# Optimization experiments

Hardware: AMD Instinct MI355X
Metric: run time of the kernel (lower is better)

The kernel has to match this reference:

```python
import jax, jax.numpy as jnp
import numpy as np

L, E, NH, V, BS = 8, 1024, 16, 32000, 1024  # layers, embed, heads, vocab, block_size
HD = E // NH  # head dim = 64
FF = 4 * E


def layernorm(x, scale, bias, eps=1e-5):
    mu = jnp.mean(x, axis=-1, keepdims=True)
    var = jnp.var(x, axis=-1, keepdims=True)
    return (x - mu) * jax.lax.rsqrt(var + eps) * scale + bias


def setup_inputs() -> dict:
    key = jax.random.key(0)
    ks = jax.random.split(key, 16)
    s = 0.02
    B, T = 2, 1024
    return {
        "idx": jax.random.randint(ks[0], (B, T), 0, V),
        "tok_emb": jax.random.normal(ks[1], (V, E), jnp.float32) * s,
        "pos_emb": jax.random.normal(ks[2], (BS, E), jnp.float32) * s,
        "Wq": jax.random.normal(ks[3], (L, E, E), jnp.float32) * s,
        "Wk": jax.random.normal(ks[4], (L, E, E), jnp.float32) * s,
        "Wv": jax.random.normal(ks[5], (L, E, E), jnp.float32) * s,
        "Wo": jax.random.normal(ks[6], (L, E, E), jnp.float32) * s,
        "bo": jnp.zeros((L, E), jnp.float32),
        "ln1_s": jnp.ones((L, E), jnp.float32),
        "ln1_b": jnp.zeros((L, E), jnp.float32),
        "W1": jax.random.normal(ks[7], (L, E, FF), jnp.float32) * s,
        "b1": jnp.zeros((L, FF), jnp.float32),
        "W2": jax.random.normal(ks[8], (L, FF, E), jnp.float32) * s,
        "b2": jnp.zeros((L, E), jnp.float32),
        "ln2_s": jnp.ones((L, E), jnp.float32),
        "ln2_b": jnp.zeros((L, E), jnp.float32),
        "lnf_s": jnp.ones((E,), jnp.float32),
        "lnf_b": jnp.zeros((E,), jnp.float32),
        "lm_w": jax.random.normal(ks[9], (E, V), jnp.float32) * s,
        "lm_b": jnp.zeros((V,), jnp.float32),
    }


def reference(idx, tok_emb, pos_emb, Wq, Wk, Wv, Wo, bo, ln1_s, ln1_b,
              W1, b1, W2, b2, ln2_s, ln2_b, lnf_s, lnf_b, lm_w, lm_b):
    B, T = idx.shape
    x = tok_emb[idx] + pos_emb[:T]  # [B,T,E]
    causal = jnp.triu(jnp.ones((T, T), bool), 1)  # True above diagonal -> masked
    scale = 1.0 / jnp.sqrt(jnp.asarray(HD, x.dtype))
    for l in range(L):
        h = layernorm(x, ln1_s[l], ln1_b[l])
        q = (h @ Wq[l]).reshape(B, T, NH, HD)
        k = (h @ Wk[l]).reshape(B, T, NH, HD)
        v = (h @ Wv[l]).reshape(B, T, NH, HD)
        scores = jnp.einsum("bthd,bshd->bhts", q, k) * scale  # [B,H,T,T]
        scores = jnp.where(causal, -jnp.inf, scores)
        attn = jax.nn.softmax(scores, axis=-1)
        o = jnp.einsum("bhts,bshd->bthd", attn, v).reshape(B, T, E)
        x = x + o @ Wo[l] + bo[l]
        h2 = layernorm(x, ln2_s[l], ln2_b[l])
        x = x + jax.nn.gelu(h2 @ W1[l] + b1[l], approximate=False) @ W2[l] + b2[l]
    x = layernorm(x, lnf_s, lnf_b)
    logits = x @ lm_w + lm_b  # [B,T,V]
    return logits
```

## Files before the change

### kernel.cpp

```cpp
#include <hip/hip_runtime.h>

#define EDIM 1024
#define NHEADS 16
#define HDIM 64
#define TSEQ 1024
#define NBATCH 2
#define MROWS 2048
#define FFDIM 4096
#define NLAYERS 8
#define VOCAB 32000
#define QKVN 3072

typedef __attribute__((ext_vector_type(4))) float f32x4;
typedef __attribute__((ext_vector_type(8))) short short8;

__device__ __forceinline__ unsigned short f2bf(float f) {
    union { float f; unsigned u; } v; v.f = f;
    unsigned r = v.u + 0x7fffu + ((v.u >> 16) & 1u);
    return (unsigned short)(r >> 16);
}

__device__ __forceinline__ f32x4 mfma_bf16(short8 a, short8 b, f32x4 c) {
    return __builtin_amdgcn_mfma_f32_16x16x32_bf16(a, b, c, 0, 0, 0);
}

__device__ __forceinline__ void gload16(const unsigned short* g, unsigned short* l) {
    __builtin_amdgcn_global_load_lds(
        (const __attribute__((address_space(1))) unsigned int*)g,
        (__attribute__((address_space(3))) unsigned int*)l, 16, 0, 0);
}

__global__ __launch_bounds__(256) void embed_kernel(
    const int* __restrict__ idx, const float* __restrict__ tok,
    const float* __restrict__ pos, float* __restrict__ x)
{
    int row = blockIdx.x;
    int t = row & (TSEQ - 1);
    int tokid = idx[row];
    const float* tp = tok + (size_t)tokid * EDIM;
    const float* pp = pos + (size_t)t * EDIM;
    float* xp = x + (size_t)row * EDIM;
    int c = threadIdx.x * 4;
    f32x4 a = *(const f32x4*)(tp + c);
    f32x4 b = *(const f32x4*)(pp + c);
    *(f32x4*)(xp + c) = a + b;
}

__device__ __forceinline__ void ln_store(
    f32x4 v, int tid, const float* __restrict__ sc, const float* __restrict__ bi,
    unsigned short* __restrict__ hrow)
{
    float sum = v[0] + v[1] + v[2] + v[3];
    float sq = v[0]*v[0] + v[1]*v[1] + v[2]*v[2] + v[3]*v[3];
    #pragma unroll
    for (int m = 1; m <= 32; m <<= 1) { sum += __shfl_xor(sum, m); sq += __shfl_xor(sq, m); }
    __shared__ float sh[8];
    int w = tid >> 6;
    if ((tid & 63) == 0) { sh[w] = sum; sh[4 + w] = sq; }
    __syncthreads();
    sum = sh[0] + sh[1] + sh[2] + sh[3];
    sq  = sh[4] + sh[5] + sh[6] + sh[7];
    float mu = sum * (1.0f / EDIM);
    float inv = rsqrtf(sq * (1.0f / EDIM) - mu * mu + 1e-5f);
    int c = tid * 4;
    unsigned o0 = (unsigned)f2bf((v[0] - mu) * inv * sc[c + 0] + bi[c + 0])
                | ((unsigned)f2bf((v[1] - mu) * inv * sc[c + 1] + bi[c + 1]) << 16);
    unsigned o1 = (unsigned)f2bf((v[2] - mu) * inv * sc[c + 2] + bi[c + 2])
                | ((unsigned)f2bf((v[3] - mu) * inv * sc[c + 3] + bi[c + 3]) << 16);
    unsigned* hp = (unsigned*)(hrow + c);
    hp[0] = o0; hp[1] = o1;
}

__global__ __launch_bounds__(256) void ln_kernel(
    const float* __restrict__ x, const float* __restrict__ sc,
    const float* __restrict__ bi, unsigned short* __restrict__ h)
{
    int row = blockIdx.x, tid = threadIdx.x;
    f32x4 v = *(const f32x4*)(x + (size_t)row * EDIM + tid * 4);
    ln_store(v, tid, sc, bi, h + (size_t)row * EDIM);
}

template<int KZ>
__global__ __launch_bounds__(256) void reduce_ln_kernel(
    const float* __restrict__ part, const float* __restrict__ bias,
    float* __restrict__ x, const float* __restrict__ sc,
    const float* __restrict__ bi, unsigned short* __restrict__ h)
{
    int row = blockIdx.x, tid = threadIdx.x;
    int c = tid * 4;
    f32x4 s = *(const f32x4*)(x + (size_t)row * EDIM + c);
    s += *(const f32x4*)(bias + c);
    #pragma unroll
    for (int kz = 0; kz < KZ; ++kz)
        s += *(const f32x4*)(part + ((size_t)kz * MROWS + row) * EDIM + c);
    *(f32x4*)(x + (size_t)row * EDIM + c) = s;
    ln_store(s, tid, sc, bi, h + (size_t)row * EDIM);
}

__device__ __forceinline__ void conv_tile(
    const float* __restrict__ W, unsigned short* __restrict__ WT,
    int Kdim, int Ndim, int k0, int n0, int tid)
{
    __shared__ unsigned short T[64][72];
    int r = tid >> 4, c4 = (tid & 15) * 4;
    #pragma unroll
    for (int i = 0; i < 4; ++i) {
        f32x4 v = *(const f32x4*)(W + (size_t)(k0 + r + 16 * i) * Ndim + n0 + c4);
        T[c4 + 0][r + 16 * i] = f2bf(v[0]);
        T[c4 + 1][r + 16 * i] = f2bf(v[1]);
        T[c4 + 2][r + 16 * i] = f2bf(v[2]);
        T[c4 + 3][r + 16 * i] = f2bf(v[3]);
    }
    __syncthreads();
    int nr = tid >> 2, kc = (tid & 3) * 16;
    short8 o0 = *(const short8*)&T[nr][kc];
    short8 o1 = *(const short8*)&T[nr][kc + 8];
    *(short8*)(WT + (size_t)(n0 + nr) * Kdim + k0 + kc)     = o0;
    *(short8*)(WT + (size_t)(n0 + nr) * Kdim + k0 + kc + 8) = o1;
}

__global__ __launch_bounds__(256) void wconv_layer_kernel(
    const float* __restrict__ Wq, const float* __restrict__ Wk,
    const float* __restrict__ Wv, const float* __restrict__ Wo,
    const float* __restrict__ W1, const float* __restrict__ W2,
    unsigned short* __restrict__ qkvT, unsigned short* __restrict__ woT,
    unsigned short* __restrict__ w1T, unsigned short* __restrict__ w2T)
{
    int bid = blockIdx.x, tid = threadIdx.x;
    if (bid < 768) {
        int wsel = bid >> 8, t = bid & 255;
        const float* src = wsel == 0 ? Wq : (wsel == 1 ? Wk : Wv);
        conv_tile(src, qkvT + (size_t)wsel * EDIM * EDIM, EDIM, EDIM,
                  (t & 15) * 64, (t >> 4) * 64, tid);
    } else if (bid < 1024) {
        int t = bid - 768;
        conv_tile(Wo, woT, EDIM, EDIM, (t & 15) * 64, (t >> 4) * 64, tid);
    } else if (bid < 2048) {
        int t = bid - 1024;
        conv_tile(W1, w1T, EDIM, FFDIM, (t & 15) * 64, (t >> 4) * 64, tid);
    } else {
        int t = bid - 2048;
        conv_tile(W2, w2T, FFDIM, EDIM, (t >> 4) * 64, (t & 15) * 64, tid);
    }
}

__global__ __launch_bounds__(256) void wconv_kernel(
    const float* __restrict__ W, unsigned short* __restrict__ WT, int Kdim, int Ndim)
{
    conv_tile(W, WT, Kdim, Ndim, blockIdx.x * 64, blockIdx.y * 64, threadIdx.x);
}

template<int EPI>
__global__ __launch_bounds__(256, 3) void gemm128(
    const unsigned short* __restrict__ A, const unsigned short* __restrict__ WT,
    const float* __restrict__ bias, float* __restrict__ Cf,
    unsigned short* __restrict__ Cb, int Ndim, int Kdim,
    int ntiles, int nwg, int kspan)
{
    __shared__ __align__(16) unsigned short A_lds[128][64];
    __shared__ __align__(16) unsigned short B_lds[128][64];
    int tid = threadIdx.x;
    int q8 = nwg >> 3;
    int swz = (int)(blockIdx.x & 7) * q8 + (int)(blockIdx.x >> 3);
    int bm0 = (swz / ntiles) * 128, bn0 = (swz % ntiles) * 128;
    int kz = blockIdx.y;
    int lane = tid & 63, w = tid >> 6;
    int wr = w >> 1, wc = w & 1;
    int r16 = lane & 15, cc = lane >> 4;
    int lrow = lane >> 3;
    int lcol = ((lane & 7) ^ lrow) * 8;
    int sw = r16 & 7;

    f32x4 acc[4][4];
    #pragma unroll
    for (int m = 0; m < 4; ++m)
        #pragma unroll
        for (int n = 0; n < 4; ++n) acc[m][n] = {0.f, 0.f, 0.f, 0.f};

    int kbeg = kz * kspan, kend = kbeg + kspan;
    for (int k0 = kbeg; k0 < kend; k0 += 64) {
        #pragma unroll
        for (int i = 0; i < 4; ++i) {
            int c = i * 4 + w;
            gload16(A + (size_t)(bm0 + c * 8 + lrow) * Kdim + k0 + lcol,
                    (unsigned short*)A_lds + c * 512);
            gload16(WT + (size_t)(bn0 + c * 8 + lrow) * Kdim + k0 + lcol,
                    (unsigned short*)B_lds + c * 512);
        }
        __syncthreads();
        #pragma unroll
        for (int kh = 0; kh < 2; ++kh) {
            short8 af[4], bfr[4];
            #pragma unroll
            for (int m = 0; m < 4; ++m)
                af[m] = *(const short8*)&A_lds[wr * 64 + m * 16 + r16][((kh * 4 + cc) ^ sw) * 8];
            #pragma unroll
            for (int n = 0; n < 4; ++n)
                bfr[n] = *(const short8*)&B_lds[wc * 64 + n * 16 + r16][((kh * 4 + cc) ^ sw) * 8];
            #pragma unroll
            for (int m = 0; m < 4; ++m)
                #pragma unroll
                for (int n = 0; n < 4; ++n)
                    acc[m][n] = mfma_bf16(af[m], bfr[n], acc[m][n]);
        }
        __syncthreads();
    }

    float* Cpart = Cf + (size_t)kz * MROWS * Ndim;
    #pragma unroll
    for (int m = 0; m < 4; ++m) {
        #pragma unroll
        for (int n = 0; n < 4; ++n) {
            #pragma unroll
            for (int j = 0; j < 4; ++j) {
                int row = bm0 + wr * 64 + m * 16 + cc * 4 + j;
                int col = bn0 + wc * 64 + n * 16 + r16;
                float vv = acc[m][n][j];
                if constexpr (EPI == 2) {
                    vv += bias[col];
                    vv = 0.5f * vv * (1.0f + erff(vv * 0.70710678118654752f));
                }
                if constexpr (EPI == 0 || EPI == 2)
                    Cb[(size_t)row * Ndim + col] = f2bf(vv);
                else
                    Cpart[(size_t)row * Ndim + col] = vv;
            }
        }
    }
}

__global__ __launch_bounds__(256, 2) void gemm_wide_lm(
    const unsigned short* __restrict__ A, const unsigned short* __restrict__ WT,
    const float* __restrict__ bias, float* __restrict__ Cf,
    int Ndim, int Kdim, int mtiles, int ntiles)
{
    __shared__ __align__(16) unsigned short A_lds[128][64];
    __shared__ __align__(16) unsigned short B_lds[256][64];
    int tid = threadIdx.x;
    int nwg = mtiles * ntiles;
    int q8 = nwg >> 3;
    int swz = (int)(blockIdx.x & 7) * q8 + (int)(blockIdx.x >> 3);
    int bn0 = (swz / mtiles) * 256, bm0 = (swz % mtiles) * 128;
    int lane = tid & 63, w = tid >> 6;
    int wr = w >> 1, wc = w & 1;
    int r16 = lane & 15, cc = lane >> 4;
    int lrow = lane >> 3;
    int lcol = ((lane & 7) ^ lrow) * 8;
    int sw = r16 & 7;

    f32x4 acc[4][8];
    #pragma unroll
    for (int m = 0; m < 4; ++m)
        #pragma unroll
        for (int n = 0; n < 8; ++n) acc[m][n] = {0.f, 0.f, 0.f, 0.f};

    for (int k0 = 0; k0 < Kdim; k0 += 64) {
        #pragma unroll
        for (int i = 0; i < 4; ++i) {
            int c = i * 4 + w;
            gload16(A + (size_t)(bm0 + c * 8 + lrow) * Kdim + k0 + lcol,
                    (unsigned short*)A_lds + c * 512);
        }
        #pragma unroll
        for (int i = 0; i < 8; ++i) {
            int c = i * 4 + w;
            gload16(WT + (size_t)(bn0 + c * 8 + lrow) * Kdim + k0 + lcol,
                    (unsigned short*)B_lds + c * 512);
        }
        __syncthreads();
        #pragma unroll
        for (int kh = 0; kh < 2; ++kh) {
            short8 af[4], bfr[8];
            #pragma unroll
            for (int m = 0; m < 4; ++m)
                af[m] = *(const short8*)&A_lds[wr * 64 + m * 16 + r16][((kh * 4 + cc) ^ sw) * 8];
            #pragma unroll
            for (int n = 0; n < 8; ++n)
                bfr[n] = *(const short8*)&B_lds[wc * 128 + n * 16 + r16][((kh * 4 + cc) ^ sw) * 8];
            #pragma unroll
            for (int m = 0; m < 4; ++m)
                #pragma unroll
                for (int n = 0; n < 8; ++n)
                    acc[m][n] = mfma_bf16(af[m], bfr[n], acc[m][n]);
        }
        __syncthreads();
    }

    #pragma unroll
    for (int m = 0; m < 4; ++m) {
        #pragma unroll
        for (int n = 0; n < 8; ++n) {
            #pragma unroll
            for (int j = 0; j < 4; ++j) {
                int row = bm0 + wr * 64 + m * 16 + cc * 4 + j;
                int col = bn0 + wc * 128 + n * 16 + r16;
                Cf[(size_t)row * Ndim + col] = acc[m][n][j] + bias[col];
            }
        }
    }
}

__global__ __launch_bounds__(256) void attn_kernel(
    const unsigned short* __restrict__ qkv, unsigned short* __restrict__ o)
{
    __shared__ __align__(16) unsigned short K_lds[64][72];
    __shared__ __align__(16) unsigned short VT_lds[64][72];
    __shared__ __align__(16) unsigned short P_lds[4][16][72];

    int qt = blockIdx.x, head = blockIdx.y, bb = blockIdx.z;
    int tid = threadIdx.x, w = tid >> 6, lane = tid & 63;
    int r16 = lane & 15, cc = lane >> 4;
    size_t base = ((size_t)bb * TSEQ) * QKVN + head * HDIM;
    const unsigned short* q = qkv + base;
    const unsigned short* k = qkv + base + EDIM;
    const unsigned short* v = qkv + base + 2 * EDIM;
    size_t obase = ((size_t)bb * TSEQ) * EDIM + head * HDIM;
    int qbase = qt * 64;

    const unsigned short* qp = q + (size_t)(qbase + w * 16 + r16) * QKVN;
    short8 aq0 = *(const short8*)(qp + cc * 8);
    short8 aq1 = *(const short8*)(qp + 32 + cc * 8);

    f32x4 oacc[4];
    float mrow[4], lrow[4];
    #pragma unroll
    for (int n = 0; n < 4; ++n) oacc[n] = {0.f, 0.f, 0.f, 0.f};
    #pragma unroll
    for (int j = 0; j < 4; ++j) { mrow[j] = -1e30f; lrow[j] = 0.f; }

    int krow = tid >> 2, kch = tid & 3;
    int vkey2 = (tid & 31) * 2, vdh = tid >> 5;

    for (int kt = 0; kt <= qt; ++kt) {
        int kbase = kt * 64;
        const unsigned short* kp = k + (size_t)(kbase + krow) * QKVN + kch * 16;
        short8 kv0 = *(const short8*)kp;
        short8 kv1 = *(const short8*)(kp + 8);
        *(short8*)&K_lds[krow][kch * 16]     = kv0;
        *(short8*)&K_lds[krow][kch * 16 + 8] = kv1;
        const unsigned short* vp0 = v + (size_t)(kbase + vkey2) * QKVN + vdh * 8;
        short8 v0 = *(const short8*)vp0;
        short8 v1 = *(const short8*)(vp0 + QKVN);
        #pragma unroll
        for (int i = 0; i < 8; ++i) {
            unsigned pk = (unsigned)(unsigned short)v0[i]
                        | ((unsigned)(unsigned short)v1[i] << 16);
            *(unsigned*)&VT_lds[vdh * 8 + i][vkey2] = pk;
        }
        __syncthreads();

        f32x4 s[4];
        #pragma unroll
        for (int n = 0; n < 4; ++n) {
            short8 bk0 = *(const short8*)&K_lds[n * 16 + r16][cc * 8];
            short8 bk1 = *(const short8*)&K_lds[n * 16 + r16][32 + cc * 8];
            f32x4 z = {0.f, 0.f, 0.f, 0.f};
            z = mfma_bf16(aq0, bk0, z);
            z = mfma_bf16(aq1, bk1, z);
            s[n] = z;
        }
        bool diag = (kt == qt);
        float p[4][4];
        #pragma unroll
        for (int n = 0; n < 4; ++n)
            #pragma unroll
            for (int j = 0; j < 4; ++j) {
                float sv = s[n][j] * 0.125f;
                if (diag && (kbase + n * 16 + r16 > qbase + w * 16 + cc * 4 + j)) sv = -1e30f;
                p[n][j] = sv;
            }
        float alpha[4];
        #pragma unroll
        for (int j = 0; j < 4; ++j) {
            float tmax = fmaxf(fmaxf(p[0][j], p[1][j]), fmaxf(p[2][j], p[3][j]));
            #pragma unroll
            for (int mm = 1; mm <= 8; mm <<= 1) tmax = fmaxf(tmax, __shfl_xor(tmax, mm));
            float mnew = fmaxf(mrow[j], tmax);
            alpha[j] = __expf(mrow[j] - mnew);
            mrow[j] = mnew;
            float tsum = 0.f;
            #pragma unroll
            for (int n = 0; n < 4; ++n) {
                float pe = __expf(p[n][j] - mnew);
                p[n][j] = pe;
                tsum += pe;
            }
            #pragma unroll
            for (int mm = 1; mm <= 8; mm <<= 1) tsum += __shfl_xor(tsum, mm);
            lrow[j] = lrow[j] * alpha[j] + tsum;
        }
        #pragma unroll
        for (int n = 0; n < 4; ++n) {
            #pragma unroll
            for (int j = 0; j < 4; ++j) {
                P_lds[w][cc * 4 + j][n * 16 + r16] = f2bf(p[n][j]);
                oacc[n][j] *= alpha[j];
            }
        }
        short8 pa0 = *(const short8*)&P_lds[w][r16][cc * 8];
        short8 pa1 = *(const short8*)&P_lds[w][r16][32 + cc * 8];
        #pragma unroll
        for (int n = 0; n < 4; ++n) {
            short8 bv0 = *(const short8*)&VT_lds[n * 16 + r16][cc * 8];
            short8 bv1 = *(const short8*)&VT_lds[n * 16 + r16][32 + cc * 8];
            oacc[n] = mfma_bf16(pa0, bv0, oacc[n]);
            oacc[n] = mfma_bf16(pa1, bv1, oacc[n]);
        }
        __syncthreads();
    }
    float rl[4];
    #pragma unroll
    for (int j = 0; j < 4; ++j) rl[j] = 1.0f / lrow[j];
    #pragma unroll
    for (int n = 0; n < 4; ++n)
        #pragma unroll
        for (int j = 0; j < 4; ++j) {
            int row = qbase + w * 16 + cc * 4 + j;
            o[obase + (size_t)row * EDIM + n * 16 + r16] = f2bf(oacc[n][j] * rl[j]);
        }
}

extern "C" void kernel_launch(void* const* d_in, const int* in_sizes, int n_in,
                              void* d_out, int out_size, void* d_ws, size_t ws_size,
                              hipStream_t stream) {
    const int*   idx     = (const int*)d_in[0];
    const float* tok_emb = (const float*)d_in[1];
    const float* pos_emb = (const float*)d_in[2];
    const float* Wq      = (const float*)d_in[3];
    const float* Wk      = (const float*)d_in[4];
    const float* Wv      = (const float*)d_in[5];
    const float* Wo      = (const float*)d_in[6];
    const float* bo      = (const float*)d_in[7];
    const float* ln1_s   = (const float*)d_in[8];
    const float* ln1_b   = (const float*)d_in[9];
    const float* W1      = (const float*)d_in[10];
    const float* b1      = (const float*)d_in[11];
    const float* W2      = (const float*)d_in[12];
    const float* b2      = (const float*)d_in[13];
    const float* ln2_s   = (const float*)d_in[14];
    const float* ln2_b   = (const float*)d_in[15];
    const float* lnf_s   = (const float*)d_in[16];
    const float* lnf_b   = (const float*)d_in[17];
    const float* lm_w    = (const float*)d_in[18];
    const float* lm_b    = (const float*)d_in[19];
    float* out = (float*)d_out;

    char* ws = (char*)d_ws;
    float*          x    = (float*)ws;
    unsigned short* h    = (unsigned short*)(ws + (8  << 20));
    unsigned short* qkv  = (unsigned short*)(ws + (12 << 20));
    unsigned short* ao   = (unsigned short*)(ws + (24 << 20));
    unsigned short* ff   = (unsigned short*)(ws + (28 << 20));
    unsigned short* qkvT = (unsigned short*)(ws + (44 << 20));
    unsigned short* woT  = (unsigned short*)(ws + (50 << 20));
    unsigned short* w1T  = (unsigned short*)(ws + (52 << 20));
    unsigned short* w2T  = (unsigned short*)(ws + (60 << 20));
    unsigned short* lmT  = (unsigned short*)(ws + (68 << 20));
    float*          part = (float*)(ws + (68 << 20));

    dim3 blk(256);
    embed_kernel<<<MROWS, blk, 0, stream>>>(idx, tok_emb, pos_emb, x);
    ln_kernel<<<MROWS, blk, 0, stream>>>(x, ln1_s, ln1_b, h);

    for (int l = 0; l < NLAYERS; ++l) {
        size_t eo = (size_t)l * EDIM * EDIM;
        wconv_layer_kernel<<<3072, blk, 0, stream>>>(
            Wq + eo, Wk + eo, Wv + eo, Wo + eo,
            W1 + (size_t)l * EDIM * FFDIM, W2 + (size_t)l * FFDIM * EDIM,
            qkvT, woT, w1T, w2T);

        gemm128<0><<<dim3(384, 1), blk, 0, stream>>>(h, qkvT, nullptr, nullptr, qkv, QKVN, EDIM, 24, 384, EDIM);
        attn_kernel<<<dim3(TSEQ / 64, NHEADS, NBATCH), blk, 0, stream>>>(qkv, ao);
        gemm128<4><<<dim3(128, 4), blk, 0, stream>>>(ao, woT, nullptr, part, nullptr, EDIM, EDIM, 8, 128, 256);
        reduce_ln_kernel<4><<<MROWS, blk, 0, stream>>>(part, bo + l * EDIM, x, ln2_s + l * EDIM, ln2_b + l * EDIM, h);
        gemm128<2><<<dim3(512, 1), blk, 0, stream>>>(h, w1T, b1 + l * FFDIM, nullptr, ff, FFDIM, EDIM, 32, 512, EDIM);
        gemm128<4><<<dim3(128, 4), blk, 0, stream>>>(ff, w2T, nullptr, part, nullptr, EDIM, FFDIM, 8, 128, 1024);
        if (l < NLAYERS - 1)
            reduce_ln_kernel<4><<<MROWS, blk, 0, stream>>>(part, b2 + l * EDIM, x, ln1_s + (l + 1) * EDIM, ln1_b + (l + 1) * EDIM, h);
        else
            reduce_ln_kernel<4><<<MROWS, blk, 0, stream>>>(part, b2 + l * EDIM, x, lnf_s, lnf_b, h);
    }
    wconv_kernel<<<dim3(16, 500), blk, 0, stream>>>(lm_w, lmT, EDIM, VOCAB);
    gemm_wide_lm<<<dim3(2000, 1), blk, 0, stream>>>(h, lmT, lm_b, out, VOCAB, EDIM, 16, 125);
}
```

Measured before the change: 1.555 ms.

## Pre-transpose V, read K/V from global in attention, replace split-K GEMMs

Adds a separate kernel that transposes V per head into a contiguous layout. Attention then reads K and V^T fragments directly from global memory with raised wave priority, dropping the LDS staging and per-tile barriers. The Wo and W2 projections move from a 4-way split-K 128x128 GEMM to a 64x128 tile GEMM with no split, so the reduce+LN kernels read one partial instead of four. This cuts partial-buffer traffic and synchronisation, at the cost of an extra launch, redundant global K/V loads across waves, and longer K loops per workgroup.

```diff
diff --git a/kernel.cpp b/kernel.cpp
--- a/kernel.cpp
+++ b/kernel.cpp
@@ -150,6 +150,33 @@
     conv_tile(W, WT, Kdim, Ndim, blockIdx.x * 64, blockIdx.y * 64, threadIdx.x);
 }
 
+__global__ __launch_bounds__(256) void vtrans_kernel(
+    const unsigned short* __restrict__ qkv, unsigned short* __restrict__ voT)
+{
+    __shared__ unsigned short T[64][72];
+    int hb = blockIdx.x, tt = blockIdx.y;
+    int head = hb >> 1, bb = hb & 1;
+    const unsigned short* v = qkv + ((size_t)bb * TSEQ) * QKVN + head * HDIM + 2 * EDIM;
+    unsigned short* dst = voT + ((size_t)(bb * NHEADS + head) * HDIM) * TSEQ;
+    int tid = threadIdx.x;
+    int tr = tid >> 2, c16 = (tid & 3) * 16;
+    const unsigned short* vp = v + (size_t)(tt * 64 + tr) * QKVN + c16;
+    short8 a0 = *(const short8*)vp;
+    short8 a1 = *(const short8*)(vp + 8);
+    *(short8*)&T[tr][c16]     = a0;
+    *(short8*)&T[tr][c16 + 8] = a1;
+    __syncthreads();
+    int dd = tid >> 2, t16 = (tid & 3) * 16;
+    short8 o0, o1;
+    #pragma unroll
+    for (int i = 0; i < 8; ++i) {
+        o0[i] = (short)T[t16 + i][dd];
+        o1[i] = (short)T[t16 + 8 + i][dd];
+    }
+    *(short8*)(dst + (size_t)dd * TSEQ + tt * 64 + t16)     = o0;
+    *(short8*)(dst + (size_t)dd * TSEQ + tt * 64 + t16 + 8) = o1;
+}
+
 template<int EPI>
 __global__ __launch_bounds__(256, 3) void gemm128(
     const unsigned short* __restrict__ A, const unsigned short* __restrict__ WT,
@@ -206,7 +233,6 @@
         __syncthreads();
     }
 
-    float* Cpart = Cf + (size_t)kz * MROWS * Ndim;
     #pragma unroll
     for (int m = 0; m < 4; ++m) {
         #pragma unroll
@@ -220,13 +246,77 @@
                     vv += bias[col];
                     vv = 0.5f * vv * (1.0f + erff(vv * 0.70710678118654752f));
                 }
-                if constexpr (EPI == 0 || EPI == 2)
-                    Cb[(size_t)row * Ndim + col] = f2bf(vv);
-                else
-                    Cpart[(size_t)row * Ndim + col] = vv;
+                Cb[(size_t)row * Ndim + col] = f2bf(vv);
             }
         }
     }
+}
+
+__global__ __launch_bounds__(256, 4) void gemm64(
+    const unsigned short* __restrict__ A, const unsigned short* __restrict__ WT,
+    float* __restrict__ Cf, int Ndim, int Kdim, int ntiles, int nwg)
+{
+    __shared__ __align__(16) unsigned short A_lds[64][64];
+    __shared__ __align__(16) unsigned short B_lds[128][64];
+    int tid = threadIdx.x;
+    int q8 = nwg >> 3;
+    int swz = (int)(blockIdx.x & 7) * q8 + (int)(blockIdx.x >> 3);
+    int bm0 = (swz / ntiles) * 64, bn0 = (swz % ntiles) * 128;
+    int lane = tid & 63, w = tid >> 6;
+    int wr = w >> 1, wc = w & 1;
+    int r16 = lane & 15, cc = lane >> 4;
+    int lrow = lane >> 3;
+    int lcol = ((lane & 7) ^ lrow) * 8;
+    int sw = r16 & 7;
+
+    f32x4 acc[2][4];
+    #pragma unroll
+    for (int m = 0; m < 2; ++m)
+        #pragma unroll
+        for (int n = 0; n < 4; ++n) acc[m][n] = {0.f, 0.f, 0.f, 0.f};
+
+    for (int k0 = 0; k0 < Kdim; k0 += 64) {
+        #pragma unroll
+        for (int i = 0; i < 2; ++i) {
+            int c = i * 4 + w;
+            gload16(A + (size_t)(bm0 + c * 8 + lrow) * Kdim + k0 + lcol,
+                    (unsigned short*)A_lds + c * 512);
+        }
+        #pragma unroll
+        for (int i = 0; i < 4; ++i) {
+            int c = i * 4 + w;
+            gload16(WT + (size_t)(bn0 + c * 8 + lrow) * Kdim + k0 + lcol,
+                    (unsigned short*)B_lds + c * 512);
+        }
+        __syncthreads();
+        #pragma unroll
+        for (int kh = 0; kh < 2; ++kh) {
+            short8 af[2], bfr[4];
+            #pragma unroll
+            for (int m = 0; m < 2; ++m)
+                af[m] = *(const short8*)&A_lds[wr * 32 + m * 16 + r16][((kh * 4 + cc) ^ sw) * 8];
+            #pragma unroll
+            for (int n = 0; n < 4; ++n)
+                bfr[n] = *(const short8*)&B_lds[wc * 64 + n * 16 + r16][((kh * 4 + cc) ^ sw) * 8];
+            #pragma unroll
+            for (int m = 0; m < 2; ++m)
+                #pragma unroll
+                for (int n = 0; n < 4; ++n)
+                    acc[m][n] = mfma_bf16(af[m], bfr[n], acc[m][n]);
+        }
+        __syncthreads();
+    }
+
+    #pragma unroll
+    for (int m = 0; m < 2; ++m)
+        #pragma unroll
+        for (int n = 0; n < 4; ++n)
+            #pragma unroll
+            for (int j = 0; j < 4; ++j) {
+                int row = bm0 + wr * 32 + m * 16 + cc * 4 + j;
+                int col = bn0 + wc * 64 + n * 16 + r16;
+                Cf[(size_t)row * Ndim + col] = acc[m][n][j];
+            }
 }
 
 __global__ __launch_bounds__(256, 2) void gemm_wide_lm(
@@ -301,19 +391,19 @@
 }
 
 __global__ __launch_bounds__(256) void attn_kernel(
-    const unsigned short* __restrict__ qkv, unsigned short* __restrict__ o)
-{
-    __shared__ __align__(16) unsigned short K_lds[64][72];
-    __shared__ __align__(16) unsigned short VT_lds[64][72];
+    const unsigned short* __restrict__ qkv, const unsigned short* __restrict__ voT,
+    unsigned short* __restrict__ o)
+{
     __shared__ __align__(16) unsigned short P_lds[4][16][72];
 
-    int qt = blockIdx.x, head = blockIdx.y, bb = blockIdx.z;
+    int hb = blockIdx.x, qt = blockIdx.y;
+    int head = hb >> 1, bb = hb & 1;
     int tid = threadIdx.x, w = tid >> 6, lane = tid & 63;
     int r16 = lane & 15, cc = lane >> 4;
     size_t base = ((size_t)bb * TSEQ) * QKVN + head * HDIM;
     const unsigned short* q = qkv + base;
     const unsigned short* k = qkv + base + EDIM;
-    const unsigned short* v = qkv + base + 2 * EDIM;
+    const unsigned short* vt = voT + ((size_t)(bb * NHEADS + head) * HDIM) * TSEQ;
     size_t obase = ((size_t)bb * TSEQ) * EDIM + head * HDIM;
     int qbase = qt * 64;
 
@@ -328,37 +418,21 @@
     #pragma unroll
     for (int j = 0; j < 4; ++j) { mrow[j] = -1e30f; lrow[j] = 0.f; }
 
-    int krow = tid >> 2, kch = tid & 3;
-    int vkey2 = (tid & 31) * 2, vdh = tid >> 5;
-
     for (int kt = 0; kt <= qt; ++kt) {
         int kbase = kt * 64;
-        const unsigned short* kp = k + (size_t)(kbase + krow) * QKVN + kch * 16;
-        short8 kv0 = *(const short8*)kp;
-        short8 kv1 = *(const short8*)(kp + 8);
-        *(short8*)&K_lds[krow][kch * 16]     = kv0;
-        *(short8*)&K_lds[krow][kch * 16 + 8] = kv1;
-        const unsigned short* vp0 = v + (size_t)(kbase + vkey2) * QKVN + vdh * 8;
-        short8 v0 = *(const short8*)vp0;
-        short8 v1 = *(const short8*)(vp0 + QKVN);
-        #pragma unroll
-        for (int i = 0; i < 8; ++i) {
-            unsigned pk = (unsigned)(unsigned short)v0[i]
-                        | ((unsigned)(unsigned short)v1[i] << 16);
-            *(unsigned*)&VT_lds[vdh * 8 + i][vkey2] = pk;
-        }
-        __syncthreads();
-
         f32x4 s[4];
+        __builtin_amdgcn_s_setprio(1);
         #pragma unroll
         for (int n = 0; n < 4; ++n) {
-            short8 bk0 = *(const short8*)&K_lds[n * 16 + r16][cc * 8];
-            short8 bk1 = *(const short8*)&K_lds[n * 16 + r16][32 + cc * 8];
+            const unsigned short* kp = k + (size_t)(kbase + n * 16 + r16) * QKVN;
+            short8 bk0 = *(const short8*)(kp + cc * 8);
+            short8 bk1 = *(const short8*)(kp + 32 + cc * 8);
             f32x4 z = {0.f, 0.f, 0.f, 0.f};
             z = mfma_bf16(aq0, bk0, z);
             z = mfma_bf16(aq1, bk1, z);
             s[n] = z;
         }
+        __builtin_amdgcn_s_setprio(0);
         bool diag = (kt == qt);
         float p[4][4];
         #pragma unroll
@@ -399,14 +473,16 @@
         }
         short8 pa0 = *(const short8*)&P_lds[w][r16][cc * 8];
         short8 pa1 = *(const short8*)&P_lds[w][r16][32 + cc * 8];
+        __builtin_amdgcn_s_setprio(1);
         #pragma unroll
         for (int n = 0; n < 4; ++n) {
-            short8 bv0 = *(const short8*)&VT_lds[n * 16 + r16][cc * 8];
-            short8 bv1 = *(const short8*)&VT_lds[n * 16 + r16][32 + cc * 8];
+            const unsigned short* vp = vt + (size_t)(n * 16 + r16) * TSEQ + kbase;
+            short8 bv0 = *(const short8*)(vp + cc * 8);
+            short8 bv1 = *(const short8*)(vp + 32 + cc * 8);
             oacc[n] = mfma_bf16(pa0, bv0, oacc[n]);
             oacc[n] = mfma_bf16(pa1, bv1, oacc[n]);
         }
-        __syncthreads();
+        __builtin_amdgcn_s_setprio(0);
     }
     float rl[4];
     #pragma unroll
@@ -457,6 +533,7 @@
     unsigned short* w2T  = (unsigned short*)(ws + (60 << 20));
     unsigned short* lmT  = (unsigned short*)(ws + (68 << 20));
     float*          part = (float*)(ws + (68 << 20));
+    unsigned short* voT  = (unsigned short*)(ws + (100 << 20));
 
     dim3 blk(256);
     embed_kernel<<<MROWS, blk, 0, stream>>>(idx, tok_emb, pos_emb, x);
@@ -470,15 +547,16 @@
             qkvT, woT, w1T, w2T);
 
         gemm128<0><<<dim3(384, 1), blk, 0, stream>>>(h, qkvT, nullptr, nullptr, qkv, QKVN, EDIM, 24, 384, EDIM);
-        attn_kernel<<<dim3(TSEQ / 64, NHEADS, NBATCH), blk, 0, stream>>>(qkv, ao);
-        gemm128<4><<<dim3(128, 4), blk, 0, stream>>>(ao, woT, nullptr, part, nullptr, EDIM, EDIM, 8, 128, 256);
-        reduce_ln_kernel<4><<<MROWS, blk, 0, stream>>>(part, bo + l * EDIM, x, ln2_s + l * EDIM, ln2_b + l * EDIM, h);
+        vtrans_kernel<<<dim3(32, 16), blk, 0, stream>>>(qkv, voT);
+        attn_kernel<<<dim3(32, 16), blk, 0, stream>>>(qkv, voT, ao);
+        gemm64<<<dim3(256, 1), blk, 0, stream>>>(ao, woT, part, EDIM, EDIM, 8, 256);
+        reduce_ln_kernel<1><<<MROWS, blk, 0, stream>>>(part, bo + l * EDIM, x, ln2_s + l * EDIM, ln2_b + l * EDIM, h);
         gemm128<2><<<dim3(512, 1), blk, 0, stream>>>(h, w1T, b1 + l * FFDIM, nullptr, ff, FFDIM, EDIM, 32, 512, EDIM);
-        gemm128<4><<<dim3(128, 4), blk, 0, stream>>>(ff, w2T, nullptr, part, nullptr, EDIM, FFDIM, 8, 128, 1024);
+        gemm64<<<dim3(256, 1), blk, 0, stream>>>(ff, w2T, part, EDIM, FFDIM, 8, 256);
         if (l < NLAYERS - 1)
-            reduce_ln_kernel<4><<<MROWS, blk, 0, stream>>>(part, b2 + l * EDIM, x, ln1_s + (l + 1) * EDIM, ln1_b + (l + 1) * EDIM, h);
+            reduce_ln_kernel<1><<<MROWS, blk, 0, stream>>>(part, b2 + l * EDIM, x, ln1_s + (l + 1) * EDIM, ln1_b + (l + 1) * EDIM, h);
         else
-            reduce_ln_kernel<4><<<MROWS, blk, 0, stream>>>(part, b2 + l * EDIM, x, lnf_s, lnf_b, h);
+            reduce_ln_kernel<1><<<MROWS, blk, 0, stream>>>(part, b2 + l * EDIM, x, lnf_s, lnf_b, h);
     }
     wconv_kernel<<<dim3(16, 500), blk, 0, stream>>>(lm_w, lmT, EDIM, VOCAB);
     gemm_wide_lm<<<dim3(2000, 1), blk, 0, stream>>>(h, lmT, lm_b, out, VOCAB, EDIM, 16, 125);
```

New measurement: 1.818 ms. 1.17x slower.

## Add triple-buffered 512-thread GEMM for FFN1 and LM head

Applied to the files above, without the earlier changes.

Replaces the single-buffered wide LM-head GEMM with a templated 128x256-tile kernel using 8 waves, a 3-stage LDS ring with async global loads, and vmcnt-based waits so loads for tile t+2 overlap MFMA work on tile t. The same kernel now also handles the FFN up-projection with a fused bias+GELU bf16 epilogue, moving it off the 128x128 gemm128 path. It also raises MFMA issue priority around the compute block. The cost is larger LDS use (about 144KB per block), which limits occupancy, and the hand-written waitcnt sequencing is fragile.

```diff
diff --git a/kernel.cpp b/kernel.cpp
--- a/kernel.cpp
+++ b/kernel.cpp
@@ -206,7 +206,6 @@
         __syncthreads();
     }
 
-    float* Cpart = Cf + (size_t)kz * MROWS * Ndim;
     #pragma unroll
     for (int m = 0; m < 4; ++m) {
         #pragma unroll
@@ -216,85 +215,111 @@
                 int row = bm0 + wr * 64 + m * 16 + cc * 4 + j;
                 int col = bn0 + wc * 64 + n * 16 + r16;
                 float vv = acc[m][n][j];
-                if constexpr (EPI == 2) {
-                    vv += bias[col];
-                    vv = 0.5f * vv * (1.0f + erff(vv * 0.70710678118654752f));
-                }
-                if constexpr (EPI == 0 || EPI == 2)
+                if constexpr (EPI == 0)
                     Cb[(size_t)row * Ndim + col] = f2bf(vv);
                 else
-                    Cpart[(size_t)row * Ndim + col] = vv;
+                    (Cf + (size_t)kz * MROWS * Ndim)[(size_t)row * Ndim + col] = vv;
             }
         }
     }
 }
 
-__global__ __launch_bounds__(256, 2) void gemm_wide_lm(
+template<int EPI>
+__global__ __launch_bounds__(512, 2) void gemm_p3(
     const unsigned short* __restrict__ A, const unsigned short* __restrict__ WT,
     const float* __restrict__ bias, float* __restrict__ Cf,
-    int Ndim, int Kdim, int mtiles, int ntiles)
-{
-    __shared__ __align__(16) unsigned short A_lds[128][64];
-    __shared__ __align__(16) unsigned short B_lds[256][64];
-    int tid = threadIdx.x;
-    int nwg = mtiles * ntiles;
-    int q8 = nwg >> 3;
-    int swz = (int)(blockIdx.x & 7) * q8 + (int)(blockIdx.x >> 3);
-    int bn0 = (swz / mtiles) * 256, bm0 = (swz % mtiles) * 128;
-    int lane = tid & 63, w = tid >> 6;
-    int wr = w >> 1, wc = w & 1;
-    int r16 = lane & 15, cc = lane >> 4;
-    int lrow = lane >> 3;
-    int lcol = ((lane & 7) ^ lrow) * 8;
-    int sw = r16 & 7;
-
-    f32x4 acc[4][8];
+    unsigned short* __restrict__ Cb, int Ndim, int Kdim, int mtiles, int ntiles)
+{
+    __shared__ __align__(16) unsigned short LDS[3][24576];
+    const int tid = threadIdx.x;
+    const int nwg = mtiles * ntiles, q8 = nwg >> 3;
+    const int swz = (int)(blockIdx.x & 7) * q8 + (int)(blockIdx.x >> 3);
+    const int bn0 = (swz / mtiles) * 256, bm0 = (swz % mtiles) * 128;
+    const int lane = tid & 63, w = tid >> 6;
+    const int wr = w >> 2, wc = w & 3;
+    const int r16 = lane & 15, cc = lane >> 4;
+    const int lrow = lane >> 3;
+    const int lcol = ((lane & 7) ^ lrow) * 8;
+    const int sw = r16 & 7;
+
+    f32x4 acc[4][4];
     #pragma unroll
     for (int m = 0; m < 4; ++m)
         #pragma unroll
-        for (int n = 0; n < 8; ++n) acc[m][n] = {0.f, 0.f, 0.f, 0.f};
-
-    for (int k0 = 0; k0 < Kdim; k0 += 64) {
+        for (int n = 0; n < 4; ++n) acc[m][n] = {0.f, 0.f, 0.f, 0.f};
+
+    const int nk = Kdim >> 6;
+
+    auto STAGE = [&](int t, int bufidx) {
+        int k0 = t * 64;
+        unsigned short* buf = &LDS[bufidx][0];
+        #pragma unroll
+        for (int i = 0; i < 2; ++i) {
+            int c = i * 8 + w;
+            gload16(A + (size_t)(bm0 + c * 8 + lrow) * Kdim + k0 + lcol, buf + c * 512);
+        }
         #pragma unroll
         for (int i = 0; i < 4; ++i) {
-            int c = i * 4 + w;
-            gload16(A + (size_t)(bm0 + c * 8 + lrow) * Kdim + k0 + lcol,
-                    (unsigned short*)A_lds + c * 512);
-        }
-        #pragma unroll
-        for (int i = 0; i < 8; ++i) {
-            int c = i * 4 + w;
-            gload16(WT + (size_t)(bn0 + c * 8 + lrow) * Kdim + k0 + lcol,
-                    (unsigned short*)B_lds + c * 512);
-        }
-        __syncthreads();
+            int c = i * 8 + w;
+            gload16(WT + (size_t)(bn0 + c * 8 + lrow) * Kdim + k0 + lcol, buf + 8192 + c * 512);
+        }
+    };
+
+    STAGE(0, 0);
+    STAGE(1, 1);
+    asm volatile("s_waitcnt vmcnt(6)" ::: "memory");
+    __builtin_amdgcn_sched_barrier(0);
+    __builtin_amdgcn_s_barrier();
+    __builtin_amdgcn_sched_barrier(0);
+
+    int cur = 0;
+    for (int t = 0; t < nk; ++t) {
+        if (t + 2 < nk) STAGE(t + 2, cur == 0 ? 2 : cur - 1);
+        const unsigned short* Abuf = &LDS[cur][0];
+        const unsigned short* Bbuf = &LDS[cur][8192];
         #pragma unroll
         for (int kh = 0; kh < 2; ++kh) {
-            short8 af[4], bfr[8];
+            short8 af[4], bfr[4];
             #pragma unroll
             for (int m = 0; m < 4; ++m)
-                af[m] = *(const short8*)&A_lds[wr * 64 + m * 16 + r16][((kh * 4 + cc) ^ sw) * 8];
-            #pragma unroll
-            for (int n = 0; n < 8; ++n)
-                bfr[n] = *(const short8*)&B_lds[wc * 128 + n * 16 + r16][((kh * 4 + cc) ^ sw) * 8];
+                af[m] = *(const short8*)&Abuf[(wr * 64 + m * 16 + r16) * 64 + ((kh * 4 + cc) ^ sw) * 8];
+            #pragma unroll
+            for (int n = 0; n < 4; ++n)
+                bfr[n] = *(const short8*)&Bbuf[(wc * 64 + n * 16 + r16) * 64 + ((kh * 4 + cc) ^ sw) * 8];
+            __builtin_amdgcn_s_setprio(1);
             #pragma unroll
             for (int m = 0; m < 4; ++m)
                 #pragma unroll
-                for (int n = 0; n < 8; ++n)
+                for (int n = 0; n < 4; ++n)
                     acc[m][n] = mfma_bf16(af[m], bfr[n], acc[m][n]);
-        }
-        __syncthreads();
+            __builtin_amdgcn_s_setprio(0);
+        }
+        if (t + 1 < nk) {
+            if (t + 2 < nk) asm volatile("s_waitcnt vmcnt(6)" ::: "memory");
+            else            asm volatile("s_waitcnt vmcnt(0)" ::: "memory");
+            __builtin_amdgcn_sched_barrier(0);
+            __builtin_amdgcn_s_barrier();
+            __builtin_amdgcn_sched_barrier(0);
+            asm volatile("" ::: "memory");
+        }
+        cur = cur == 2 ? 0 : cur + 1;
     }
 
     #pragma unroll
     for (int m = 0; m < 4; ++m) {
         #pragma unroll
-        for (int n = 0; n < 8; ++n) {
+        for (int n = 0; n < 4; ++n) {
             #pragma unroll
             for (int j = 0; j < 4; ++j) {
                 int row = bm0 + wr * 64 + m * 16 + cc * 4 + j;
-                int col = bn0 + wc * 128 + n * 16 + r16;
-                Cf[(size_t)row * Ndim + col] = acc[m][n][j] + bias[col];
+                int col = bn0 + wc * 64 + n * 16 + r16;
+                float vv = acc[m][n][j] + bias[col];
+                if constexpr (EPI == 2) {
+                    vv = 0.5f * vv * (1.0f + erff(vv * 0.70710678118654752f));
+                    Cb[(size_t)row * Ndim + col] = f2bf(vv);
+                } else {
+                    Cf[(size_t)row * Ndim + col] = vv;
+                }
             }
         }
     }
@@ -473,7 +498,7 @@
         attn_kernel<<<dim3(TSEQ / 64, NHEADS, NBATCH), blk, 0, stream>>>(qkv, ao);
         gemm128<4><<<dim3(128, 4), blk, 0, stream>>>(ao, woT, nullptr, part, nullptr, EDIM, EDIM, 8, 128, 256);
         reduce_ln_kernel<4><<<MROWS, blk, 0, stream>>>(part, bo + l * EDIM, x, ln2_s + l * EDIM, ln2_b + l * EDIM, h);
-        gemm128<2><<<dim3(512, 1), blk, 0, stream>>>(h, w1T, b1 + l * FFDIM, nullptr, ff, FFDIM, EDIM, 32, 512, EDIM);
+        gemm_p3<2><<<dim3(256, 1), dim3(512), 0, stream>>>(h, w1T, b1 + l * FFDIM, nullptr, ff, FFDIM, EDIM, 16, 16);
         gemm128<4><<<dim3(128, 4), blk, 0, stream>>>(ff, w2T, nullptr, part, nullptr, EDIM, FFDIM, 8, 128, 1024);
         if (l < NLAYERS - 1)
             reduce_ln_kernel<4><<<MROWS, blk, 0, stream>>>(part, b2 + l * EDIM, x, ln1_s + (l + 1) * EDIM, ln1_b + (l + 1) * EDIM, h);
@@ -481,5 +506,5 @@
             reduce_ln_kernel<4><<<MROWS, blk, 0, stream>>>(part, b2 + l * EDIM, x, lnf_s, lnf_b, h);
     }
     wconv_kernel<<<dim3(16, 500), blk, 0, stream>>>(lm_w, lmT, EDIM, VOCAB);
-    gemm_wide_lm<<<dim3(2000, 1), blk, 0, stream>>>(h, lmT, lm_b, out, VOCAB, EDIM, 16, 125);
-}
+    gemm_p3<3><<<dim3(2000, 1), dim3(512), 0, stream>>>(h, lmT, lm_b, out, nullptr, VOCAB, EDIM, 16, 125);
+}
```

New measurement: 1.550 ms. No clear change (-0.3%).
